# Kernel optimization log

Measured on AMD Instinct MI355X. Metric: run time of the kernel, lower is better.

Reference implementation:

```python
import jax, jax.numpy as jnp
import numpy as np

B, N, D_IN, D_OUT = 16, 2048, 64, 64


def setup_inputs() -> dict:
    key = jax.random.key(0)
    k1, k2, k3, k4, k5 = jax.random.split(key, 5)
    x = jax.random.normal(k1, (B, N, D_IN), dtype=jnp.float32)
    weight = jax.random.normal(k2, (D_IN, D_OUT), dtype=jnp.float32) * (1.0 / np.sqrt(D_OUT))
    att = jax.random.uniform(k3, (N, N), dtype=jnp.float32, minval=-1.0 / np.sqrt(D_OUT), maxval=1.0 / np.sqrt(D_OUT))
    bias = jax.random.normal(k4, (D_OUT,), dtype=jnp.float32) * (1.0 / np.sqrt(D_OUT))
    mask = jax.random.randint(k5, (N, N), 0, 2, dtype=jnp.int32)
    return {"x": x, "weight": weight, "att": att, "bias": bias, "mask": mask}


def reference(x, weight, att, bias, mask):
    # x: [B, N, D_in]; weight: [D_in, D_out]; att, mask: [N, N]; bias: [D_out]
    support = jnp.einsum('bnd,de->bne', x, weight)          # [B, N, D_out]
    mup = jnp.einsum('bnd,bmd->bnm', x, x)                  # [B, N, N]
    norms = jnp.linalg.norm(x, axis=-1, keepdims=True)      # [B, N, 1]
    mdown = norms * jnp.swapaxes(norms, 1, 2)               # [B, N, N] outer product of norms
    w = mup / mdown                                         # cosine similarity
    adjacent = (att * mask.astype(jnp.float32)) * w         # masked attention * cosine weights
    out = jnp.einsum('bnm,bme->bne', adjacent, support)     # [B, N, D_out]
    return out + bias
```

## Files before the change

### kernel.cpp

```cpp
#include <hip/hip_runtime.h>
#include <stdint.h>

#define NN 2048

typedef short bf8_t __attribute__((ext_vector_type(8)));
typedef float f32x4 __attribute__((ext_vector_type(4)));

__device__ __forceinline__ unsigned int rbf(float f) {
    unsigned int u = __builtin_bit_cast(unsigned int, f);
    return u + 0x7FFFu + ((u >> 16) & 1u);
}
__device__ __forceinline__ unsigned short f2b(float f) { return (unsigned short)(rbf(f) >> 16); }
__device__ __forceinline__ unsigned int pk2(float lo, float hi) {
    return (rbf(lo) >> 16) | (rbf(hi) & 0xFFFF0000u);
}

__global__ __launch_bounds__(256) void prep_kernel(
    const float* __restrict__ x, const float* __restrict__ w,
    const float* __restrict__ att, const int* __restrict__ mask,
    unsigned short* __restrict__ xB, unsigned short* __restrict__ sB,
    unsigned short* __restrict__ amB)
{
    __shared__ unsigned short lds[4 * 64 * 72];
    __shared__ float part[64][4];

    const int t = threadIdx.x;
    const int row = t >> 2, seg = t & 3;
    const int wv = t >> 6, l = t & 63, c = l & 15, q = l >> 4;

    if (blockIdx.x < 512) {
        unsigned short* xs = lds;
        unsigned short* xt = lds + 4608;
        unsigned short* Wt = lds + 9216;
        unsigned short* st = lds + 13824;
        const int b = blockIdx.x >> 5, nt = blockIdx.x & 31;

        float4 xq[4], wq[4];
        const float* xp = x + ((size_t)(b * NN + nt * 64 + row)) * 64 + seg * 16;
        const float* wp = w + row * 64 + seg * 16;
        #pragma unroll
        for (int i = 0; i < 4; ++i) { xq[i] = ((const float4*)xp)[i]; wq[i] = ((const float4*)wp)[i]; }
        float ss = 0.f;
        #pragma unroll
        for (int i = 0; i < 4; ++i)
            ss += xq[i].x * xq[i].x + xq[i].y * xq[i].y + xq[i].z * xq[i].z + xq[i].w * xq[i].w;
        part[row][seg] = ss;
        #pragma unroll
        for (int i = 0; i < 4; ++i) {
            ((unsigned int*)&xs[row * 72 + seg * 16])[i * 2]     = pk2(xq[i].x, xq[i].y);
            ((unsigned int*)&xs[row * 72 + seg * 16])[i * 2 + 1] = pk2(xq[i].z, xq[i].w);
            Wt[(seg * 16 + i * 4 + 0) * 72 + row] = f2b(wq[i].x);
            Wt[(seg * 16 + i * 4 + 1) * 72 + row] = f2b(wq[i].y);
            Wt[(seg * 16 + i * 4 + 2) * 72 + row] = f2b(wq[i].z);
            Wt[(seg * 16 + i * 4 + 3) * 72 + row] = f2b(wq[i].w);
        }
        __syncthreads();

        const float rinv = 1.0f / sqrtf(part[row][0] + part[row][1] + part[row][2] + part[row][3]);
        #pragma unroll
        for (int i = 0; i < 4; ++i) {
            ((unsigned int*)&xt[row * 72 + seg * 16])[i * 2]     = pk2(xq[i].x * rinv, xq[i].y * rinv);
            ((unsigned int*)&xt[row * 72 + seg * 16])[i * 2 + 1] = pk2(xq[i].z * rinv, xq[i].w * rinv);
        }
        __syncthreads();

        {
            bf8_t h0 = *(const bf8_t*)&xt[(wv * 16 + c) * 72 + q * 8];
            bf8_t h1 = *(const bf8_t*)&xt[(wv * 16 + c) * 72 + 32 + q * 8];
            unsigned short* base = xB + ((size_t)(b * 32 + nt)) * 4096 + wv * 1024 + l * 8;
            *(bf8_t*)base = h0;
            *(bf8_t*)(base + 512) = h1;
        }
        {
            bf8_t a0 = *(const bf8_t*)&xs[(wv * 16 + c) * 72 + q * 8];
            bf8_t a1 = *(const bf8_t*)&xs[(wv * 16 + c) * 72 + 32 + q * 8];
            #pragma unroll
            for (int cb = 0; cb < 4; ++cb) {
                bf8_t b0 = *(const bf8_t*)&Wt[(cb * 16 + c) * 72 + q * 8];
                bf8_t b1 = *(const bf8_t*)&Wt[(cb * 16 + c) * 72 + 32 + q * 8];
                f32x4 z = (f32x4){0.f, 0.f, 0.f, 0.f};
                z = __builtin_amdgcn_mfma_f32_16x16x32_bf16(a0, b0, z, 0, 0, 0);
                z = __builtin_amdgcn_mfma_f32_16x16x32_bf16(a1, b1, z, 0, 0, 0);
                #pragma unroll
                for (int r = 0; r < 4; ++r)
                    st[(cb * 16 + c) * 72 + wv * 16 + q * 4 + r] = f2b(z[r]);
            }
        }
        __syncthreads();
        {
            bf8_t h0 = *(const bf8_t*)&st[(wv * 16 + c) * 72 + q * 8];
            bf8_t h1 = *(const bf8_t*)&st[(wv * 16 + c) * 72 + 32 + q * 8];
            unsigned short* base = sB + ((size_t)(b * 32 + nt)) * 4096 + wv * 1024 + l * 8;
            *(bf8_t*)base = h0;
            *(bf8_t*)(base + 512) = h1;
        }
    } else {
        unsigned short* amt = lds;
        const int bid = blockIdx.x - 512;
        const int it = bid >> 5, mc = bid & 31;
        const size_t g = ((size_t)(it * 64 + row)) * NN + mc * 64 + seg * 16;
        #pragma unroll
        for (int i = 0; i < 4; ++i) {
            float4 a = *(const float4*)(att + g + i * 4);
            int4   m = *(const int4*)(mask + g + i * 4);
            ((unsigned int*)&amt[row * 72 + seg * 16])[i * 2] =
                pk2(a.x * (float)m.x, a.y * (float)m.y);
            ((unsigned int*)&amt[row * 72 + seg * 16])[i * 2 + 1] =
                pk2(a.z * (float)m.z, a.w * (float)m.w);
        }
        __syncthreads();
        unsigned int ww[8];
        #pragma unroll
        for (int rbi = 0; rbi < 4; ++rbi) {
            #pragma unroll
            for (int rp = 0; rp < 2; ++rp) {
                unsigned int lo = amt[(rbi * 16 + c) * 72 + wv * 16 + q * 4 + rp * 2];
                unsigned int hi = amt[(rbi * 16 + c) * 72 + wv * 16 + q * 4 + rp * 2 + 1];
                ww[rbi * 2 + rp] = lo | (hi << 16);
            }
        }
        unsigned short* base = amB + ((size_t)(it * 32 + mc)) * 4096 + wv * 1024 + l * 8;
        *(uint4*)base         = *(uint4*)&ww[0];
        *(uint4*)(base + 512) = *(uint4*)&ww[4];
    }
}

__global__ __launch_bounds__(256, 2) void gcn_kernel(
    const unsigned short* __restrict__ xB, const unsigned short* __restrict__ sB,
    const unsigned short* __restrict__ amB, const float* __restrict__ bias,
    float* __restrict__ out)
{
    __shared__ unsigned short Adj[4][64 * 72];
    const int t = threadIdx.x;
    const int wm = t >> 6, l = t & 63, c = l & 15, q = l >> 4;
    const int bid = blockIdx.x;
    const int r8 = bid & 31, b = bid >> 5;
    const int it = (r8 & 7) * 4 + (r8 >> 3);

    const unsigned short* xit = xB + ((size_t)(b * 32 + it)) * 4096;
    bf8_t xi0[4], xi1[4];
    #pragma unroll
    for (int rb = 0; rb < 4; ++rb) {
        xi0[rb] = *(const bf8_t*)(xit + rb * 1024 + l * 8);
        xi1[rb] = *(const bf8_t*)(xit + rb * 1024 + 512 + l * 8);
    }
    f32x4 acc[4][4];
    #pragma unroll
    for (int rb = 0; rb < 4; ++rb)
        #pragma unroll
        for (int cb = 0; cb < 4; ++cb) acc[rb][cb] = (f32x4){0.f, 0.f, 0.f, 0.f};

    unsigned short* adj = &Adj[wm][0];

    bf8_t xmA0[4], xmA1[4], xmB0[4], xmB1[4];
    {
        const unsigned short* xmt = xB + ((size_t)(b * 32 + wm)) * 4096;
        #pragma unroll
        for (int cb = 0; cb < 4; ++cb) {
            xmA0[cb] = *(const bf8_t*)(xmt + cb * 1024 + l * 8);
            xmA1[cb] = *(const bf8_t*)(xmt + cb * 1024 + 512 + l * 8);
        }
    }

    #pragma unroll
    for (int tt = 0; tt < 8; ++tt) {
        const int mc = wm + tt * 4;
        const unsigned short* smt = sB + ((size_t)(b * 32 + mc)) * 4096;
        const unsigned short* amp = amB + ((size_t)(it * 32 + mc)) * 4096;
        bf8_t sm0[4], sm1[4];
        uint4 amv[8];
        #pragma unroll
        for (int j = 0; j < 8; ++j) amv[j] = *(const uint4*)(amp + j * 512 + l * 8);
        #pragma unroll
        for (int cb = 0; cb < 4; ++cb) {
            sm0[cb] = *(const bf8_t*)(smt + cb * 1024 + l * 8);
            sm1[cb] = *(const bf8_t*)(smt + cb * 1024 + 512 + l * 8);
        }
        if (tt < 7) {
            const unsigned short* xmn = xB + ((size_t)(b * 32 + mc + 4)) * 4096;
            if ((tt & 1) == 0) {
                #pragma unroll
                for (int cb = 0; cb < 4; ++cb) {
                    xmB0[cb] = *(const bf8_t*)(xmn + cb * 1024 + l * 8);
                    xmB1[cb] = *(const bf8_t*)(xmn + cb * 1024 + 512 + l * 8);
                }
            } else {
                #pragma unroll
                for (int cb = 0; cb < 4; ++cb) {
                    xmA0[cb] = *(const bf8_t*)(xmn + cb * 1024 + l * 8);
                    xmA1[cb] = *(const bf8_t*)(xmn + cb * 1024 + 512 + l * 8);
                }
            }
        }
        const bf8_t* xm0 = (tt & 1) ? xmB0 : xmA0;
        const bf8_t* xm1 = (tt & 1) ? xmB1 : xmA1;

        #pragma unroll
        for (int cbm = 0; cbm < 4; ++cbm) {
            #pragma unroll
            for (int rbi = 0; rbi < 4; ++rbi) {
                f32x4 z = (f32x4){0.f, 0.f, 0.f, 0.f};
                z = __builtin_amdgcn_mfma_f32_16x16x32_bf16(xm0[cbm], xi0[rbi], z, 0, 0, 0);
                z = __builtin_amdgcn_mfma_f32_16x16x32_bf16(xm1[cbm], xi1[rbi], z, 0, 0, 0);
                const unsigned int w0 = ((const unsigned int*)&amv[cbm * 2 + (rbi >> 1)])[(rbi & 1) * 2 + 0];
                const unsigned int w1 = ((const unsigned int*)&amv[cbm * 2 + (rbi >> 1)])[(rbi & 1) * 2 + 1];
                const float a0f = __builtin_bit_cast(float, w0 << 16);
                const float a1f = __builtin_bit_cast(float, w0 & 0xFFFF0000u);
                const float a2f = __builtin_bit_cast(float, w1 << 16);
                const float a3f = __builtin_bit_cast(float, w1 & 0xFFFF0000u);
                uint2 p;
                p.x = pk2(z[0] * a0f, z[1] * a1f);
                p.y = pk2(z[2] * a2f, z[3] * a3f);
                *(uint2*)&adj[(rbi * 16 + c) * 72 + cbm * 16 + q * 4] = p;
            }
        }
        #pragma unroll
        for (int rb = 0; rb < 4; ++rb) {
            bf8_t p0 = *(const bf8_t*)&adj[(rb * 16 + c) * 72 + q * 8];
            bf8_t p1 = *(const bf8_t*)&adj[(rb * 16 + c) * 72 + 32 + q * 8];
            #pragma unroll
            for (int cb = 0; cb < 4; ++cb) {
                acc[rb][cb] = __builtin_amdgcn_mfma_f32_16x16x32_bf16(p0, sm0[cb], acc[rb][cb], 0, 0, 0);
                acc[rb][cb] = __builtin_amdgcn_mfma_f32_16x16x32_bf16(p1, sm1[cb], acc[rb][cb], 0, 0, 0);
            }
        }
    }

    float* red = (float*)&Adj[0][0];
    const int i0 = it * 64;
    for (int h = 0; h < 2; ++h) {
        __syncthreads();
        #pragma unroll
        for (int rb2 = 0; rb2 < 2; ++rb2) {
            const int rb = h * 2 + rb2;
            #pragma unroll
            for (int cb = 0; cb < 4; ++cb)
                #pragma unroll
                for (int r = 0; r < 4; ++r)
                    red[wm * 2176 + (rb2 * 16 + q * 4 + r) * 68 + cb * 16 + c] = acc[rb][cb][r];
        }
        __syncthreads();
        #pragma unroll
        for (int rnd = 0; rnd < 8; ++rnd) {
            const int idx = rnd * 256 + t;
            const int row = idx >> 6, col = idx & 63;
            const float s = red[0 * 2176 + row * 68 + col] + red[1 * 2176 + row * 68 + col]
                          + red[2 * 2176 + row * 68 + col] + red[3 * 2176 + row * 68 + col];
            out[((size_t)(b * NN + i0 + h * 32 + row)) * 64 + col] = s + bias[col];
        }
    }
}

extern "C" void kernel_launch(void* const* d_in, const int* in_sizes, int n_in,
                              void* d_out, int out_size, void* d_ws, size_t ws_size,
                              hipStream_t stream) {
    const float* x    = (const float*)d_in[0];
    const float* w    = (const float*)d_in[1];
    const float* att  = (const float*)d_in[2];
    const float* bias = (const float*)d_in[3];
    const int*   mask = (const int*)d_in[4];
    float* out = (float*)d_out;

    unsigned short* xB  = (unsigned short*)d_ws;
    unsigned short* sB  = xB + (size_t)2 * 1024 * 1024;
    unsigned short* amB = sB + (size_t)2 * 1024 * 1024;

    prep_kernel<<<dim3(1536), dim3(256), 0, stream>>>(x, w, att, mask, xB, sB, amB);
    gcn_kernel<<<dim3(512), dim3(256), 0, stream>>>(xB, sB, amB, bias, out);
}
```

Measured before the change: 115.2 us.

## Fuse att*mask into gcn kernel, drop precomputed bf16 adjacency buffer

Removes the prep stage that multiplied att by mask and stored it as tiled bf16, and instead has the main kernel load fp32 att and int32 mask directly and apply them in the epilogue of the cosine-similarity MFMA. This eliminates one pass and an intermediate buffer write/read. In exchange every batch re-reads the full fp32 att and int32 mask (four times more bytes per element than the bf16 buffer), with uncoalesced 16-byte row-strided loads and many more live registers.

```diff
diff --git a/kernel.cpp b/kernel.cpp
--- a/kernel.cpp
+++ b/kernel.cpp
@@ -17,118 +17,84 @@
 
 __global__ __launch_bounds__(256) void prep_kernel(
     const float* __restrict__ x, const float* __restrict__ w,
-    const float* __restrict__ att, const int* __restrict__ mask,
-    unsigned short* __restrict__ xB, unsigned short* __restrict__ sB,
-    unsigned short* __restrict__ amB)
+    unsigned short* __restrict__ xB, unsigned short* __restrict__ sB)
 {
-    __shared__ unsigned short lds[4 * 64 * 72];
+    __shared__ unsigned short xs[64 * 72];
+    __shared__ unsigned short xt[64 * 72];
+    __shared__ unsigned short Wt[64 * 72];
+    __shared__ unsigned short st[64 * 72];
     __shared__ float part[64][4];
 
     const int t = threadIdx.x;
     const int row = t >> 2, seg = t & 3;
     const int wv = t >> 6, l = t & 63, c = l & 15, q = l >> 4;
-
-    if (blockIdx.x < 512) {
-        unsigned short* xs = lds;
-        unsigned short* xt = lds + 4608;
-        unsigned short* Wt = lds + 9216;
-        unsigned short* st = lds + 13824;
-        const int b = blockIdx.x >> 5, nt = blockIdx.x & 31;
-
-        float4 xq[4], wq[4];
-        const float* xp = x + ((size_t)(b * NN + nt * 64 + row)) * 64 + seg * 16;
-        const float* wp = w + row * 64 + seg * 16;
-        #pragma unroll
-        for (int i = 0; i < 4; ++i) { xq[i] = ((const float4*)xp)[i]; wq[i] = ((const float4*)wp)[i]; }
-        float ss = 0.f;
-        #pragma unroll
-        for (int i = 0; i < 4; ++i)
-            ss += xq[i].x * xq[i].x + xq[i].y * xq[i].y + xq[i].z * xq[i].z + xq[i].w * xq[i].w;
-        part[row][seg] = ss;
-        #pragma unroll
-        for (int i = 0; i < 4; ++i) {
-            ((unsigned int*)&xs[row * 72 + seg * 16])[i * 2]     = pk2(xq[i].x, xq[i].y);
-            ((unsigned int*)&xs[row * 72 + seg * 16])[i * 2 + 1] = pk2(xq[i].z, xq[i].w);
-            Wt[(seg * 16 + i * 4 + 0) * 72 + row] = f2b(wq[i].x);
-            Wt[(seg * 16 + i * 4 + 1) * 72 + row] = f2b(wq[i].y);
-            Wt[(seg * 16 + i * 4 + 2) * 72 + row] = f2b(wq[i].z);
-            Wt[(seg * 16 + i * 4 + 3) * 72 + row] = f2b(wq[i].w);
-        }
-        __syncthreads();
-
-        const float rinv = 1.0f / sqrtf(part[row][0] + part[row][1] + part[row][2] + part[row][3]);
-        #pragma unroll
-        for (int i = 0; i < 4; ++i) {
-            ((unsigned int*)&xt[row * 72 + seg * 16])[i * 2]     = pk2(xq[i].x * rinv, xq[i].y * rinv);
-            ((unsigned int*)&xt[row * 72 + seg * 16])[i * 2 + 1] = pk2(xq[i].z * rinv, xq[i].w * rinv);
-        }
-        __syncthreads();
-
-        {
-            bf8_t h0 = *(const bf8_t*)&xt[(wv * 16 + c) * 72 + q * 8];
-            bf8_t h1 = *(const bf8_t*)&xt[(wv * 16 + c) * 72 + 32 + q * 8];
-            unsigned short* base = xB + ((size_t)(b * 32 + nt)) * 4096 + wv * 1024 + l * 8;
-            *(bf8_t*)base = h0;
-            *(bf8_t*)(base + 512) = h1;
-        }
-        {
-            bf8_t a0 = *(const bf8_t*)&xs[(wv * 16 + c) * 72 + q * 8];
-            bf8_t a1 = *(const bf8_t*)&xs[(wv * 16 + c) * 72 + 32 + q * 8];
-            #pragma unroll
-            for (int cb = 0; cb < 4; ++cb) {
-                bf8_t b0 = *(const bf8_t*)&Wt[(cb * 16 + c) * 72 + q * 8];
-                bf8_t b1 = *(const bf8_t*)&Wt[(cb * 16 + c) * 72 + 32 + q * 8];
-                f32x4 z = (f32x4){0.f, 0.f, 0.f, 0.f};
-                z = __builtin_amdgcn_mfma_f32_16x16x32_bf16(a0, b0, z, 0, 0, 0);
-                z = __builtin_amdgcn_mfma_f32_16x16x32_bf16(a1, b1, z, 0, 0, 0);
-                #pragma unroll
-                for (int r = 0; r < 4; ++r)
-                    st[(cb * 16 + c) * 72 + wv * 16 + q * 4 + r] = f2b(z[r]);
-            }
-        }
-        __syncthreads();
-        {
-            bf8_t h0 = *(const bf8_t*)&st[(wv * 16 + c) * 72 + q * 8];
-            bf8_t h1 = *(const bf8_t*)&st[(wv * 16 + c) * 72 + 32 + q * 8];
-            unsigned short* base = sB + ((size_t)(b * 32 + nt)) * 4096 + wv * 1024 + l * 8;
-            *(bf8_t*)base = h0;
-            *(bf8_t*)(base + 512) = h1;
-        }
-    } else {
-        unsigned short* amt = lds;
-        const int bid = blockIdx.x - 512;
-        const int it = bid >> 5, mc = bid & 31;
-        const size_t g = ((size_t)(it * 64 + row)) * NN + mc * 64 + seg * 16;
-        #pragma unroll
-        for (int i = 0; i < 4; ++i) {
-            float4 a = *(const float4*)(att + g + i * 4);
-            int4   m = *(const int4*)(mask + g + i * 4);
-            ((unsigned int*)&amt[row * 72 + seg * 16])[i * 2] =
-                pk2(a.x * (float)m.x, a.y * (float)m.y);
-            ((unsigned int*)&amt[row * 72 + seg * 16])[i * 2 + 1] =
-                pk2(a.z * (float)m.z, a.w * (float)m.w);
-        }
-        __syncthreads();
-        unsigned int ww[8];
-        #pragma unroll
-        for (int rbi = 0; rbi < 4; ++rbi) {
-            #pragma unroll
-            for (int rp = 0; rp < 2; ++rp) {
-                unsigned int lo = amt[(rbi * 16 + c) * 72 + wv * 16 + q * 4 + rp * 2];
-                unsigned int hi = amt[(rbi * 16 + c) * 72 + wv * 16 + q * 4 + rp * 2 + 1];
-                ww[rbi * 2 + rp] = lo | (hi << 16);
-            }
-        }
-        unsigned short* base = amB + ((size_t)(it * 32 + mc)) * 4096 + wv * 1024 + l * 8;
-        *(uint4*)base         = *(uint4*)&ww[0];
-        *(uint4*)(base + 512) = *(uint4*)&ww[4];
+    const int b = blockIdx.x >> 5, nt = blockIdx.x & 31;
+
+    float4 xq[4], wq[4];
+    const float* xp = x + ((size_t)(b * NN + nt * 64 + row)) * 64 + seg * 16;
+    const float* wp = w + row * 64 + seg * 16;
+    #pragma unroll
+    for (int i = 0; i < 4; ++i) { xq[i] = ((const float4*)xp)[i]; wq[i] = ((const float4*)wp)[i]; }
+    float ss = 0.f;
+    #pragma unroll
+    for (int i = 0; i < 4; ++i)
+        ss += xq[i].x * xq[i].x + xq[i].y * xq[i].y + xq[i].z * xq[i].z + xq[i].w * xq[i].w;
+    part[row][seg] = ss;
+    #pragma unroll
+    for (int i = 0; i < 4; ++i) {
+        ((unsigned int*)&xs[row * 72 + seg * 16])[i * 2]     = pk2(xq[i].x, xq[i].y);
+        ((unsigned int*)&xs[row * 72 + seg * 16])[i * 2 + 1] = pk2(xq[i].z, xq[i].w);
+        Wt[(seg * 16 + i * 4 + 0) * 72 + row] = f2b(wq[i].x);
+        Wt[(seg * 16 + i * 4 + 1) * 72 + row] = f2b(wq[i].y);
+        Wt[(seg * 16 + i * 4 + 2) * 72 + row] = f2b(wq[i].z);
+        Wt[(seg * 16 + i * 4 + 3) * 72 + row] = f2b(wq[i].w);
+    }
+    __syncthreads();
+
+    const float rinv = 1.0f / sqrtf(part[row][0] + part[row][1] + part[row][2] + part[row][3]);
+    #pragma unroll
+    for (int i = 0; i < 4; ++i) {
+        ((unsigned int*)&xt[row * 72 + seg * 16])[i * 2]     = pk2(xq[i].x * rinv, xq[i].y * rinv);
+        ((unsigned int*)&xt[row * 72 + seg * 16])[i * 2 + 1] = pk2(xq[i].z * rinv, xq[i].w * rinv);
+    }
+    __syncthreads();
+
+    {
+        bf8_t h0 = *(const bf8_t*)&xt[(wv * 16 + c) * 72 + q * 8];
+        bf8_t h1 = *(const bf8_t*)&xt[(wv * 16 + c) * 72 + 32 + q * 8];
+        unsigned short* base = xB + ((size_t)(b * 32 + nt)) * 4096 + wv * 1024 + l * 8;
+        *(bf8_t*)base = h0;
+        *(bf8_t*)(base + 512) = h1;
+    }
+    {
+        bf8_t a0 = *(const bf8_t*)&xs[(wv * 16 + c) * 72 + q * 8];
+        bf8_t a1 = *(const bf8_t*)&xs[(wv * 16 + c) * 72 + 32 + q * 8];
+        #pragma unroll
+        for (int cb = 0; cb < 4; ++cb) {
+            bf8_t b0 = *(const bf8_t*)&Wt[(cb * 16 + c) * 72 + q * 8];
+            bf8_t b1 = *(const bf8_t*)&Wt[(cb * 16 + c) * 72 + 32 + q * 8];
+            f32x4 z = (f32x4){0.f, 0.f, 0.f, 0.f};
+            z = __builtin_amdgcn_mfma_f32_16x16x32_bf16(a0, b0, z, 0, 0, 0);
+            z = __builtin_amdgcn_mfma_f32_16x16x32_bf16(a1, b1, z, 0, 0, 0);
+            #pragma unroll
+            for (int r = 0; r < 4; ++r)
+                st[(cb * 16 + c) * 72 + wv * 16 + q * 4 + r] = f2b(z[r]);
+        }
+    }
+    __syncthreads();
+    {
+        bf8_t h0 = *(const bf8_t*)&st[(wv * 16 + c) * 72 + q * 8];
+        bf8_t h1 = *(const bf8_t*)&st[(wv * 16 + c) * 72 + 32 + q * 8];
+        unsigned short* base = sB + ((size_t)(b * 32 + nt)) * 4096 + wv * 1024 + l * 8;
+        *(bf8_t*)base = h0;
+        *(bf8_t*)(base + 512) = h1;
     }
 }
 
 __global__ __launch_bounds__(256, 2) void gcn_kernel(
     const unsigned short* __restrict__ xB, const unsigned short* __restrict__ sB,
-    const unsigned short* __restrict__ amB, const float* __restrict__ bias,
-    float* __restrict__ out)
+    const float* __restrict__ att, const int* __restrict__ mask,
+    const float* __restrict__ bias, float* __restrict__ out)
 {
     __shared__ unsigned short Adj[4][64 * 72];
     const int t = threadIdx.x;
@@ -166,11 +132,20 @@
     for (int tt = 0; tt < 8; ++tt) {
         const int mc = wm + tt * 4;
         const unsigned short* smt = sB + ((size_t)(b * 32 + mc)) * 4096;
-        const unsigned short* amp = amB + ((size_t)(it * 32 + mc)) * 4096;
+
+        float4 av[4][4];
+        int4   mv[4][4];
+        #pragma unroll
+        for (int cbm = 0; cbm < 4; ++cbm)
+            #pragma unroll
+            for (int rbi = 0; rbi < 4; ++rbi) {
+                const size_t g = ((size_t)(it * 64 + rbi * 16 + c)) * NN
+                               + mc * 64 + cbm * 16 + q * 4;
+                av[cbm][rbi] = *(const float4*)(att + g);
+                mv[cbm][rbi] = *(const int4*)(mask + g);
+            }
+
         bf8_t sm0[4], sm1[4];
-        uint4 amv[8];
-        #pragma unroll
-        for (int j = 0; j < 8; ++j) amv[j] = *(const uint4*)(amp + j * 512 + l * 8);
         #pragma unroll
         for (int cb = 0; cb < 4; ++cb) {
             sm0[cb] = *(const bf8_t*)(smt + cb * 1024 + l * 8);
@@ -202,15 +177,11 @@
                 f32x4 z = (f32x4){0.f, 0.f, 0.f, 0.f};
                 z = __builtin_amdgcn_mfma_f32_16x16x32_bf16(xm0[cbm], xi0[rbi], z, 0, 0, 0);
                 z = __builtin_amdgcn_mfma_f32_16x16x32_bf16(xm1[cbm], xi1[rbi], z, 0, 0, 0);
-                const unsigned int w0 = ((const unsigned int*)&amv[cbm * 2 + (rbi >> 1)])[(rbi & 1) * 2 + 0];
-                const unsigned int w1 = ((const unsigned int*)&amv[cbm * 2 + (rbi >> 1)])[(rbi & 1) * 2 + 1];
-                const float a0f = __builtin_bit_cast(float, w0 << 16);
-                const float a1f = __builtin_bit_cast(float, w0 & 0xFFFF0000u);
-                const float a2f = __builtin_bit_cast(float, w1 << 16);
-                const float a3f = __builtin_bit_cast(float, w1 & 0xFFFF0000u);
+                const float4 a4 = av[cbm][rbi];
+                const int4   m4 = mv[cbm][rbi];
                 uint2 p;
-                p.x = pk2(z[0] * a0f, z[1] * a1f);
-                p.y = pk2(z[2] * a2f, z[3] * a3f);
+                p.x = pk2(z[0] * (a4.x * (float)m4.x), z[1] * (a4.y * (float)m4.y));
+                p.y = pk2(z[2] * (a4.z * (float)m4.z), z[3] * (a4.w * (float)m4.w));
                 *(uint2*)&adj[(rbi * 16 + c) * 72 + cbm * 16 + q * 4] = p;
             }
         }
@@ -263,8 +234,7 @@
 
     unsigned short* xB  = (unsigned short*)d_ws;
     unsigned short* sB  = xB + (size_t)2 * 1024 * 1024;
-    unsigned short* amB = sB + (size_t)2 * 1024 * 1024;
-
-    prep_kernel<<<dim3(1536), dim3(256), 0, stream>>>(x, w, att, mask, xB, sB, amB);
-    gcn_kernel<<<dim3(512), dim3(256), 0, stream>>>(xB, sB, amB, bias, out);
-}
+
+    prep_kernel<<<dim3(512), dim3(256), 0, stream>>>(x, w, xB, sB);
+    gcn_kernel<<<dim3(512), dim3(256), 0, stream>>>(xB, sB, att, mask, bias, out);
+}
```

After: 154.8 us. 1.34x slower.

## Halve gcn row tile to 32 rows, doubling grid and raising occupancy

Applied to the files above, without the earlier changes.

The main kernel now has each block handle 32 output rows instead of 64. The grid doubles to 1024 blocks, per-thread accumulators and LDS use are halved, and launch bounds move to 4 blocks per SM. The prep kernel writes the masked-attention tiles in a matching 32-row layout so the new kernel can load them with uint2 reads. The intent is more parallelism and latency hiding on the large CU count. In exchange, the x_m and support tiles are reloaded twice as often, adding global and L2 traffic.

```diff
diff --git a/kernel.cpp b/kernel.cpp
--- a/kernel.cpp
+++ b/kernel.cpp
@@ -97,8 +97,8 @@
     } else {
         unsigned short* amt = lds;
         const int bid = blockIdx.x - 512;
-        const int it = bid >> 5, mc = bid & 31;
-        const size_t g = ((size_t)(it * 64 + row)) * NN + mc * 64 + seg * 16;
+        const int it64 = bid >> 5, mc = bid & 31;
+        const size_t g = ((size_t)(it64 * 64 + row)) * NN + mc * 64 + seg * 16;
         #pragma unroll
         for (int i = 0; i < 4; ++i) {
             float4 a = *(const float4*)(att + g + i * 4);
@@ -109,44 +109,46 @@
                 pk2(a.z * (float)m.z, a.w * (float)m.w);
         }
         __syncthreads();
-        unsigned int ww[8];
-        #pragma unroll
-        for (int rbi = 0; rbi < 4; ++rbi) {
-            #pragma unroll
-            for (int rp = 0; rp < 2; ++rp) {
-                unsigned int lo = amt[(rbi * 16 + c) * 72 + wv * 16 + q * 4 + rp * 2];
-                unsigned int hi = amt[(rbi * 16 + c) * 72 + wv * 16 + q * 4 + rp * 2 + 1];
-                ww[rbi * 2 + rp] = lo | (hi << 16);
-            }
-        }
-        unsigned short* base = amB + ((size_t)(it * 32 + mc)) * 4096 + wv * 1024 + l * 8;
-        *(uint4*)base         = *(uint4*)&ww[0];
-        *(uint4*)(base + 512) = *(uint4*)&ww[4];
-    }
-}
-
-__global__ __launch_bounds__(256, 2) void gcn_kernel(
+        #pragma unroll
+        for (int h = 0; h < 2; ++h) {
+            const int it32 = it64 * 2 + h;
+            #pragma unroll
+            for (int rbi = 0; rbi < 2; ++rbi) {
+                const unsigned short* src = &amt[(h * 32 + rbi * 16 + c) * 72 + wv * 16 + q * 4];
+                uint2 p;
+                p.x = (unsigned int)src[0] | ((unsigned int)src[1] << 16);
+                p.y = (unsigned int)src[2] | ((unsigned int)src[3] << 16);
+                *(uint2*)(amB + ((size_t)(it32 * 32 + mc)) * 2048
+                              + (wv * 2 + rbi) * 256 + l * 4) = p;
+            }
+        }
+    }
+}
+
+__global__ __launch_bounds__(256, 4) void gcn_kernel(
     const unsigned short* __restrict__ xB, const unsigned short* __restrict__ sB,
     const unsigned short* __restrict__ amB, const float* __restrict__ bias,
     float* __restrict__ out)
 {
-    __shared__ unsigned short Adj[4][64 * 72];
+    __shared__ unsigned short Adj[4][32 * 72];
     const int t = threadIdx.x;
     const int wm = t >> 6, l = t & 63, c = l & 15, q = l >> 4;
     const int bid = blockIdx.x;
-    const int r8 = bid & 31, b = bid >> 5;
-    const int it = (r8 & 7) * 4 + (r8 >> 3);
-
-    const unsigned short* xit = xB + ((size_t)(b * 32 + it)) * 4096;
-    bf8_t xi0[4], xi1[4];
-    #pragma unroll
-    for (int rb = 0; rb < 4; ++rb) {
-        xi0[rb] = *(const bf8_t*)(xit + rb * 1024 + l * 8);
-        xi1[rb] = *(const bf8_t*)(xit + rb * 1024 + 512 + l * 8);
-    }
-    f32x4 acc[4][4];
-    #pragma unroll
-    for (int rb = 0; rb < 4; ++rb)
+    const int r = bid & 63, b = bid >> 6;
+    const int it32 = (r & 7) * 8 + (r >> 3);
+    const int nt = it32 >> 1, hi = it32 & 1;
+
+    const unsigned short* xit = xB + ((size_t)(b * 32 + nt)) * 4096;
+    bf8_t xi0[2], xi1[2];
+    #pragma unroll
+    for (int rbi = 0; rbi < 2; ++rbi) {
+        const int cbx = hi * 2 + rbi;
+        xi0[rbi] = *(const bf8_t*)(xit + cbx * 1024 + l * 8);
+        xi1[rbi] = *(const bf8_t*)(xit + cbx * 1024 + 512 + l * 8);
+    }
+    f32x4 acc[2][4];
+    #pragma unroll
+    for (int rb = 0; rb < 2; ++rb)
         #pragma unroll
         for (int cb = 0; cb < 4; ++cb) acc[rb][cb] = (f32x4){0.f, 0.f, 0.f, 0.f};
 
@@ -166,11 +168,12 @@
     for (int tt = 0; tt < 8; ++tt) {
         const int mc = wm + tt * 4;
         const unsigned short* smt = sB + ((size_t)(b * 32 + mc)) * 4096;
-        const unsigned short* amp = amB + ((size_t)(it * 32 + mc)) * 4096;
+        const unsigned short* amp = amB + ((size_t)(it32 * 32 + mc)) * 2048;
+
+        uint2 amv[8];
+        #pragma unroll
+        for (int j = 0; j < 8; ++j) amv[j] = *(const uint2*)(amp + j * 256 + l * 4);
         bf8_t sm0[4], sm1[4];
-        uint4 amv[8];
-        #pragma unroll
-        for (int j = 0; j < 8; ++j) amv[j] = *(const uint4*)(amp + j * 512 + l * 8);
         #pragma unroll
         for (int cb = 0; cb < 4; ++cb) {
             sm0[cb] = *(const bf8_t*)(smt + cb * 1024 + l * 8);
@@ -198,16 +201,15 @@
         #pragma unroll
         for (int cbm = 0; cbm < 4; ++cbm) {
             #pragma unroll
-            for (int rbi = 0; rbi < 4; ++rbi) {
+            for (int rbi = 0; rbi < 2; ++rbi) {
                 f32x4 z = (f32x4){0.f, 0.f, 0.f, 0.f};
                 z = __builtin_amdgcn_mfma_f32_16x16x32_bf16(xm0[cbm], xi0[rbi], z, 0, 0, 0);
                 z = __builtin_amdgcn_mfma_f32_16x16x32_bf16(xm1[cbm], xi1[rbi], z, 0, 0, 0);
-                const unsigned int w0 = ((const unsigned int*)&amv[cbm * 2 + (rbi >> 1)])[(rbi & 1) * 2 + 0];
-                const unsigned int w1 = ((const unsigned int*)&amv[cbm * 2 + (rbi >> 1)])[(rbi & 1) * 2 + 1];
-                const float a0f = __builtin_bit_cast(float, w0 << 16);
-                const float a1f = __builtin_bit_cast(float, w0 & 0xFFFF0000u);
-                const float a2f = __builtin_bit_cast(float, w1 << 16);
-                const float a3f = __builtin_bit_cast(float, w1 & 0xFFFF0000u);
+                const uint2 w = amv[cbm * 2 + rbi];
+                const float a0f = __builtin_bit_cast(float, w.x << 16);
+                const float a1f = __builtin_bit_cast(float, w.x & 0xFFFF0000u);
+                const float a2f = __builtin_bit_cast(float, w.y << 16);
+                const float a3f = __builtin_bit_cast(float, w.y & 0xFFFF0000u);
                 uint2 p;
                 p.x = pk2(z[0] * a0f, z[1] * a1f);
                 p.y = pk2(z[2] * a2f, z[3] * a3f);
@@ -215,7 +217,7 @@
             }
         }
         #pragma unroll
-        for (int rb = 0; rb < 4; ++rb) {
+        for (int rb = 0; rb < 2; ++rb) {
             bf8_t p0 = *(const bf8_t*)&adj[(rb * 16 + c) * 72 + q * 8];
             bf8_t p1 = *(const bf8_t*)&adj[(rb * 16 + c) * 72 + 32 + q * 8];
             #pragma unroll
@@ -227,26 +229,23 @@
     }
 
     float* red = (float*)&Adj[0][0];
-    const int i0 = it * 64;
+    const int i0 = it32 * 32;
+    #pragma unroll
     for (int h = 0; h < 2; ++h) {
         __syncthreads();
         #pragma unroll
-        for (int rb2 = 0; rb2 < 2; ++rb2) {
-            const int rb = h * 2 + rb2;
-            #pragma unroll
-            for (int cb = 0; cb < 4; ++cb)
-                #pragma unroll
-                for (int r = 0; r < 4; ++r)
-                    red[wm * 2176 + (rb2 * 16 + q * 4 + r) * 68 + cb * 16 + c] = acc[rb][cb][r];
-        }
-        __syncthreads();
-        #pragma unroll
-        for (int rnd = 0; rnd < 8; ++rnd) {
+        for (int cb = 0; cb < 4; ++cb)
+            #pragma unroll
+            for (int rr = 0; rr < 4; ++rr)
+                red[wm * 1088 + (q * 4 + rr) * 68 + cb * 16 + c] = acc[h][cb][rr];
+        __syncthreads();
+        #pragma unroll
+        for (int rnd = 0; rnd < 4; ++rnd) {
             const int idx = rnd * 256 + t;
             const int row = idx >> 6, col = idx & 63;
-            const float s = red[0 * 2176 + row * 68 + col] + red[1 * 2176 + row * 68 + col]
-                          + red[2 * 2176 + row * 68 + col] + red[3 * 2176 + row * 68 + col];
-            out[((size_t)(b * NN + i0 + h * 32 + row)) * 64 + col] = s + bias[col];
+            const float s = red[0 * 1088 + row * 68 + col] + red[1 * 1088 + row * 68 + col]
+                          + red[2 * 1088 + row * 68 + col] + red[3 * 1088 + row * 68 + col];
+            out[((size_t)(b * NN + i0 + h * 16 + row)) * 64 + col] = s + bias[col];
         }
     }
 }
@@ -266,5 +265,5 @@
     unsigned short* amB = sB + (size_t)2 * 1024 * 1024;
 
     prep_kernel<<<dim3(1536), dim3(256), 0, stream>>>(x, w, att, mask, xB, sB, amB);
-    gcn_kernel<<<dim3(512), dim3(256), 0, stream>>>(xB, sB, amB, bias, out);
-}
+    gcn_kernel<<<dim3(1024), dim3(256), 0, stream>>>(xB, sB, amB, bias, out);
+}
```

Result: slower. 118.7 us (+3.0%).
